# Kernel optimization log

Measured on AMD Instinct MI355X. Metric: run time of the kernel, lower is better.

Reference implementation:

```python
import jax, jax.numpy as jnp
import numpy as np

N_NODES = 50000
N_EDGES = 800000
D = 128
N_GRAPHS = 64
N_CLASSES = 10


def setup_inputs() -> dict:
    key = jax.random.key(0)
    ks = jax.random.split(key, 10)
    x = jax.random.normal(ks[0], (N_NODES, D), dtype=jnp.float32)
    edge_index = jax.random.randint(ks[1], (2, N_EDGES), 0, N_NODES, dtype=jnp.int64)
    batch = jnp.sort(jax.random.randint(ks[2], (N_NODES,), 0, N_GRAPHS, dtype=jnp.int64))
    s = 1.0 / np.sqrt(D)
    W1a = jax.random.uniform(ks[3], (D, D), jnp.float32, -s, s)
    W1b = jax.random.uniform(ks[4], (D, D), jnp.float32, -s, s)
    W2a = jax.random.uniform(ks[5], (D, D), jnp.float32, -s, s)
    W2b = jax.random.uniform(ks[6], (D, D), jnp.float32, -s, s)
    Wfc = jax.random.uniform(ks[7], (D, N_CLASSES), jnp.float32, -s, s)
    return {
        "x": x, "edge_index": edge_index, "batch": batch,
        "W1a": W1a, "b1a": jnp.zeros((D,), jnp.float32),
        "W1b": W1b, "b1b": jnp.zeros((D,), jnp.float32),
        "W2a": W2a, "b2a": jnp.zeros((D,), jnp.float32),
        "W2b": W2b, "b2b": jnp.zeros((D,), jnp.float32),
        "Wfc": Wfc, "bfc": jnp.zeros((N_CLASSES,), jnp.float32),
    }


def _gin_conv(x, src, dst, Wa, ba, Wb, bb):
    # sum aggregation of neighbor messages x[src] into dst (eps = 0)
    agg = jax.ops.segment_sum(x[src], dst, num_segments=N_NODES)
    h = x + agg  # (1 + eps) * x + sum_{j->i} x_j
    h = jax.nn.relu(h @ Wa + ba)
    h = jax.nn.relu(h @ Wb + bb)
    return h


def reference(x, edge_index, batch, W1a, b1a, W1b, b1b, W2a, b2a, W2b, b2b, Wfc, bfc):
    src, dst = edge_index[0], edge_index[1]
    h = _gin_conv(x, src, dst, W1a, b1a, W1b, b1b)
    h = _gin_conv(h, src, dst, W2a, b2a, W2b, b2b)
    # global mean pool over graphs
    sums = jax.ops.segment_sum(h, batch, num_segments=N_GRAPHS)
    counts = jax.ops.segment_sum(jnp.ones((h.shape[0], 1), h.dtype), batch, num_segments=N_GRAPHS)
    pooled = sums / jnp.maximum(counts, 1.0)
    logits = pooled @ Wfc + bfc
    return jax.nn.sigmoid(logits)
```

## Files before the change

kernel.cpp:

```cpp
#include <hip/hip_runtime.h>

#define NN 50000
#define NE 800000
#define DF 128
#define NG 64
#define NC 10
#define NBK 98
#define PART_CHUNK 4096
#define PART_GRID 196
#define ACAP 12288
#define FINE_CAP 12288
#define RT 136

typedef short bf16x8 __attribute__((ext_vector_type(8)));
typedef float f32x4  __attribute__((ext_vector_type(4)));

__device__ __forceinline__ void atomAddF(float* p, float v) {
  __hip_atomic_fetch_add(p, v, __ATOMIC_RELAXED, __HIP_MEMORY_SCOPE_AGENT);
}
__device__ __forceinline__ float b2f(unsigned short u) {
  union { unsigned int i; float f; } v; v.i = (unsigned int)u << 16; return v.f;
}
__device__ __forceinline__ unsigned int f2b(float f) {
  unsigned int i = __float_as_uint(f);
  return (i + 0x7fffu + ((i >> 16) & 1u)) >> 16;
}

__global__ __launch_bounds__(256) void k_cast(const float* __restrict__ x,
                                              unsigned short* __restrict__ xb)
{
  const int i = blockIdx.x * 256 + threadIdx.x;
  if (i * 4 >= NN * DF) return;
  const float4 v = reinterpret_cast<const float4*>(x)[i];
  uint2 o;
  o.x = f2b(v.x) | (f2b(v.y) << 16);
  o.y = f2b(v.z) | (f2b(v.w) << 16);
  reinterpret_cast<uint2*>(xb)[i] = o;
}

__global__ __launch_bounds__(256) void k_prepw(const float* __restrict__ W0,
                                               const float* __restrict__ W1,
                                               const float* __restrict__ W2,
                                               const float* __restrict__ W3,
                                               unsigned short* __restrict__ Wt)
{
  const int o = blockIdx.x * 256 + threadIdx.x;
  if (o >= 4 * 2048) return;
  const int mat = o >> 11;
  const float* W = (mat == 0) ? W0 : (mat == 1) ? W1 : (mat == 2) ? W2 : W3;
  const int rem = o & 2047;
  const int kb = rem >> 7;
  const int n  = rem & 127;
  unsigned int u[8];
#pragma unroll
  for (int j = 0; j < 8; ++j) u[j] = f2b(W[(size_t)(kb * 8 + j) * DF + n]);
  uint4 p;
  p.x = u[0] | (u[1] << 16);
  p.y = u[2] | (u[3] << 16);
  p.z = u[4] | (u[5] << 16);
  p.w = u[6] | (u[7] << 16);
  *reinterpret_cast<uint4*>(Wt + (size_t)mat * DF * DF + (size_t)rem * 8) = p;
}

__global__ __launch_bounds__(256) void k_part(const int* __restrict__ src,
                                              const int* __restrict__ dst,
                                              int* __restrict__ cnt_b,
                                              unsigned int* __restrict__ arena)
{
  __shared__ unsigned int stage[PART_CHUNK];
  __shared__ int lhist[128], lcnt[128], lcur[128], gbase[128];
  const int tid = threadIdx.x;
  const int e0  = blockIdx.x * PART_CHUNK;
  const int nE  = min(PART_CHUNK, NE - e0);

  for (int i = tid; i < 128; i += 256) lhist[i] = 0;
  __syncthreads();

  unsigned int pk[16];
  int bk[16];
#pragma unroll
  for (int i = 0; i < 16; ++i) {
    const int e = e0 + i * 256 + tid;
    if (e < NE) {
      const int d = dst[e];
      const int s = src[e];
      const int b = d >> 9;
      bk[i] = b;
      pk[i] = ((unsigned int)b << 25) | ((unsigned int)(d & 511) << 16) | (unsigned int)s;
      atomicAdd(&lhist[b], 1);
    } else {
      bk[i] = -1;
    }
  }
  __syncthreads();
  for (int i = tid; i < 128; i += 256) lcnt[i] = lhist[i];
  __syncthreads();
  for (int off = 1; off < 128; off <<= 1) {
    int v = 0;
    if (tid < 128 && tid >= off) v = lhist[tid - off];
    __syncthreads();
    if (tid < 128) lhist[tid] += v;
    __syncthreads();
  }
  if (tid < 128) lcur[tid] = lhist[tid] - lcnt[tid];
  __syncthreads();
#pragma unroll
  for (int i = 0; i < 16; ++i) {
    if (bk[i] >= 0) {
      const int pos = atomicAdd(&lcur[bk[i]], 1);
      stage[pos] = pk[i];
    }
  }
  __syncthreads();
  if (tid < NBK) {
    const int c = lcnt[tid];
    if (c > 0) gbase[tid] = atomicAdd(&cnt_b[tid], c);
  }
  __syncthreads();
  for (int idx = tid; idx < nE; idx += 256) {
    const unsigned int p = stage[idx];
    const int b = (int)(p >> 25);
    const int loff = lhist[b] - lcnt[b];
    arena[(size_t)b * ACAP + gbase[b] + (idx - loff)] = p;
  }
}

__global__ __launch_bounds__(128) void k_bscan(const int* __restrict__ cnt_b,
                                               int* __restrict__ base_b,
                                               int* __restrict__ rs)
{
  __shared__ int sm[128];
  const int t = threadIdx.x;
  const int v = (t < NBK) ? cnt_b[t] : 0;
  sm[t] = v;
  __syncthreads();
  for (int off = 1; off < 128; off <<= 1) {
    int u = (t >= off) ? sm[t - off] : 0;
    __syncthreads();
    sm[t] += u;
    __syncthreads();
  }
  base_b[t] = sm[t] - v;
  if (t == NBK - 1) rs[NN] = sm[t];
}

__global__ __launch_bounds__(256) void k_fine(const unsigned int* __restrict__ arena,
                                              const int* __restrict__ cnt_b,
                                              const int* __restrict__ base_b,
                                              int* __restrict__ rs,
                                              unsigned short* __restrict__ es)
{
  __shared__ unsigned short les[FINE_CAP];
  __shared__ int bins[4096];
  __shared__ int partials[256];
  const int tid   = threadIdx.x;
  const int b     = blockIdx.x;
  const int cnt   = cnt_b[b];
  const int wbase = base_b[b];
  const int nbase = b << 9;
  const int nwin  = min(512, NN - nbase);
  const unsigned int* ap = arena + (size_t)b * ACAP;

  for (int i = tid; i < 4096; i += 256) bins[i] = 0;
  __syncthreads();
  for (int idx = tid; idx < cnt; idx += 256) {
    const unsigned int p = ap[idx];
    const int key = (int)(((p >> 16) & 511) << 3) | (int)((p & 0xffffu) >> 13);
    atomicAdd(&bins[key], 1);
  }
  __syncthreads();
  const int b16 = tid * 16;
  int sum = 0;
#pragma unroll
  for (int k = 0; k < 16; ++k) sum += bins[b16 + k];
  partials[tid] = sum;
  __syncthreads();
  for (int off = 1; off < 256; off <<= 1) {
    int u = (tid >= off) ? partials[tid - off] : 0;
    __syncthreads();
    partials[tid] += u;
    __syncthreads();
  }
  int run = partials[tid] - sum;
#pragma unroll
  for (int k = 0; k < 16; ++k) {
    const int v = bins[b16 + k];
    bins[b16 + k] = run;
    run += v;
  }
  __syncthreads();
  for (int i = tid; i < nwin; i += 256) rs[nbase + i] = wbase + bins[i << 3];
  __syncthreads();
  if (cnt <= FINE_CAP) {
    for (int idx = tid; idx < cnt; idx += 256) {
      const unsigned int p = ap[idx];
      const int key = (int)(((p >> 16) & 511) << 3) | (int)((p & 0xffffu) >> 13);
      const int pos = atomicAdd(&bins[key], 1);
      les[pos] = (unsigned short)(p & 0xffffu);
    }
    __syncthreads();
    for (int i = tid; i < cnt; i += 256) es[wbase + i] = les[i];
  } else {
    for (int idx = tid; idx < cnt; idx += 256) {
      const unsigned int p = ap[idx];
      const int key = (int)(((p >> 16) & 511) << 3) | (int)((p & 0xffffu) >> 13);
      const int pos = atomicAdd(&bins[key], 1);
      es[wbase + pos] = (unsigned short)(p & 0xffffu);
    }
  }
}

__global__ __launch_bounds__(256) void k_gather(const unsigned short* __restrict__ feat,
                                                unsigned short* __restrict__ outp,
                                                const int* __restrict__ rs,
                                                const unsigned short* __restrict__ es)
{
  const int wid  = (blockIdx.x * 256 + threadIdx.x) >> 6;
  const int lane = threadIdx.x & 63;
  if (wid >= NN) return;
  const int beg = rs[wid];
  const int end = rs[wid + 1];
  const int off = lane * 2;

  const unsigned int self = *reinterpret_cast<const unsigned int*>(feat + (size_t)wid * DF + off);
  float ax = b2f(self & 0xffff), ay = b2f(self >> 16);
  int j = beg;
  while (j < end && (j & 3)) {
    const int s = es[j];
    const unsigned int u = *reinterpret_cast<const unsigned int*>(feat + (size_t)s * DF + off);
    ax += b2f(u & 0xffff);
    ay += b2f(u >> 16);
    ++j;
  }
  for (; j + 3 < end; j += 4) {
    const uint2 e4 = *reinterpret_cast<const uint2*>(es + j);
    const int s0 = (int)(e4.x & 0xffffu), s1 = (int)(e4.x >> 16);
    const int s2 = (int)(e4.y & 0xffffu), s3 = (int)(e4.y >> 16);
    const unsigned int u0 = *reinterpret_cast<const unsigned int*>(feat + (size_t)s0 * DF + off);
    const unsigned int u1 = *reinterpret_cast<const unsigned int*>(feat + (size_t)s1 * DF + off);
    const unsigned int u2 = *reinterpret_cast<const unsigned int*>(feat + (size_t)s2 * DF + off);
    const unsigned int u3 = *reinterpret_cast<const unsigned int*>(feat + (size_t)s3 * DF + off);
    ax += b2f(u0 & 0xffff) + b2f(u1 & 0xffff) + b2f(u2 & 0xffff) + b2f(u3 & 0xffff);
    ay += b2f(u0 >> 16)    + b2f(u1 >> 16)    + b2f(u2 >> 16)    + b2f(u3 >> 16);
  }
  for (; j < end; ++j) {
    const int s = es[j];
    const unsigned int u = *reinterpret_cast<const unsigned int*>(feat + (size_t)s * DF + off);
    ax += b2f(u & 0xffff);
    ay += b2f(u >> 16);
  }
  const unsigned int o = f2b(ax) | (f2b(ay) << 16);
  *reinterpret_cast<unsigned int*>(outp + (size_t)wid * DF + off) = o;
}

__global__ __launch_bounds__(512) void k_gemm2(const unsigned short* __restrict__ Ab,
                                               const unsigned short* __restrict__ Wta,
                                               const float* __restrict__ ba,
                                               const unsigned short* __restrict__ Wtb,
                                               const float* __restrict__ bb,
                                               unsigned short* __restrict__ outb, int M)
{
  __shared__ unsigned short WbL[2048 * 8];
  __shared__ unsigned short hL[8][16 * RT];
  const int tid  = threadIdx.x;
  const int lane = tid & 63;
  const int w    = tid >> 6;
  const int col  = lane & 15;
  const int kq   = lane >> 4;

  for (int i = tid; i < 2048; i += 512)
    *reinterpret_cast<uint4*>(&WbL[i * 8]) =
        *reinterpret_cast<const uint4*>(&Wtb[(size_t)i * 8]);

  bf16x8 wfa[8][4];
#pragma unroll
  for (int nf = 0; nf < 8; ++nf)
#pragma unroll
    for (int s = 0; s < 4; ++s)
      wfa[nf][s] = *reinterpret_cast<const bf16x8*>(
          Wta + ((size_t)(s * 4 + kq) * 128 + nf * 16 + col) * 8);

  float4 bva[8], bvb[8];
#pragma unroll
  for (int nf = 0; nf < 8; ++nf) {
    bva[nf] = *reinterpret_cast<const float4*>(ba + nf * 16 + kq * 4);
    bvb[nf] = *reinterpret_cast<const float4*>(bb + nf * 16 + kq * 4);
  }

  __syncthreads();

  unsigned short* hw = &hL[w][0];
  const int m   = blockIdx.x * 128 + w * 16 + col;
  const int mld = (m < M) ? m : (M - 1);

  bf16x8 bc[4];
#pragma unroll
  for (int s = 0; s < 4; ++s)
    bc[s] = *reinterpret_cast<const bf16x8*>(Ab + (size_t)mld * DF + s * 32 + kq * 8);

  f32x4 acc[8];
#pragma unroll
  for (int nf = 0; nf < 8; ++nf) acc[nf] = (f32x4){0.f, 0.f, 0.f, 0.f};
#pragma unroll
  for (int s = 0; s < 4; ++s)
#pragma unroll
    for (int nf = 0; nf < 8; ++nf)
      acc[nf] = __builtin_amdgcn_mfma_f32_16x16x32_bf16(wfa[nf][s], bc[s], acc[nf], 0, 0, 0);

#pragma unroll
  for (int nf = 0; nf < 8; ++nf) {
    uint2 pk;
    pk.x = f2b(fmaxf(acc[nf][0] + bva[nf].x, 0.f)) | (f2b(fmaxf(acc[nf][1] + bva[nf].y, 0.f)) << 16);
    pk.y = f2b(fmaxf(acc[nf][2] + bva[nf].z, 0.f)) | (f2b(fmaxf(acc[nf][3] + bva[nf].w, 0.f)) << 16);
    *reinterpret_cast<uint2*>(&hw[col * RT + nf * 16 + kq * 4]) = pk;
  }
  asm volatile("s_waitcnt lgkmcnt(0)" ::: "memory");
  __builtin_amdgcn_sched_barrier(0);

  f32x4 acc2[8];
#pragma unroll
  for (int nf = 0; nf < 8; ++nf) acc2[nf] = (f32x4){0.f, 0.f, 0.f, 0.f};
#pragma unroll
  for (int s = 0; s < 4; ++s) {
    const bf16x8 hb = *reinterpret_cast<const bf16x8*>(&hw[col * RT + s * 32 + kq * 8]);
#pragma unroll
    for (int nf = 0; nf < 8; ++nf) {
      const bf16x8 wb = *reinterpret_cast<const bf16x8*>(
          &WbL[((s * 4 + kq) * 128 + nf * 16 + col) * 8]);
      acc2[nf] = __builtin_amdgcn_mfma_f32_16x16x32_bf16(wb, hb, acc2[nf], 0, 0, 0);
    }
  }
  if (m < M) {
#pragma unroll
    for (int nf = 0; nf < 8; ++nf) {
      ushort4 p;
      p.x = (unsigned short)f2b(fmaxf(acc2[nf][0] + bvb[nf].x, 0.f));
      p.y = (unsigned short)f2b(fmaxf(acc2[nf][1] + bvb[nf].y, 0.f));
      p.z = (unsigned short)f2b(fmaxf(acc2[nf][2] + bvb[nf].z, 0.f));
      p.w = (unsigned short)f2b(fmaxf(acc2[nf][3] + bvb[nf].w, 0.f));
      *reinterpret_cast<ushort4*>(outb + (size_t)m * DF + nf * 16 + kq * 4) = p;
    }
  }
}

__global__ __launch_bounds__(256) void k_pool(const unsigned short* __restrict__ h,
                                              const int* __restrict__ batch,
                                              float* __restrict__ sums,
                                              int* __restrict__ cnts)
{
  const int wv   = (blockIdx.x * 256 + threadIdx.x) >> 6;
  const int lane = threadIdx.x & 63;
  const int n0 = wv * 32;
  if (n0 >= NN) return;
  const int n1 = min(n0 + 32, NN);
  const int off = lane * 2;

  const int gfirst = batch[n0];
  const int glast  = batch[n1 - 1];
  float ax = 0.f, ay = 0.f;

  if (gfirst == glast) {
#pragma unroll 4
    for (int i = n0; i < n1; ++i) {
      const unsigned int u = *reinterpret_cast<const unsigned int*>(h + (size_t)i * DF + off);
      ax += b2f(u & 0xffff);
      ay += b2f(u >> 16);
    }
    atomAddF(&sums[gfirst * DF + off],     ax);
    atomAddF(&sums[gfirst * DF + off + 1], ay);
    if (lane == 0) atomicAdd(&cnts[gfirst], n1 - n0);
  } else {
    int g = gfirst, cnt = 0;
    for (int i = n0; i < n1; ++i) {
      const int gi = batch[i];
      if (gi != g) {
        atomAddF(&sums[g * DF + off],     ax);
        atomAddF(&sums[g * DF + off + 1], ay);
        if (lane == 0) atomicAdd(&cnts[g], cnt);
        ax = 0.f; ay = 0.f; cnt = 0; g = gi;
      }
      const unsigned int u = *reinterpret_cast<const unsigned int*>(h + (size_t)i * DF + off);
      ax += b2f(u & 0xffff);
      ay += b2f(u >> 16);
      ++cnt;
    }
    atomAddF(&sums[g * DF + off],     ax);
    atomAddF(&sums[g * DF + off + 1], ay);
    if (lane == 0) atomicAdd(&cnts[g], cnt);
  }
}

__global__ __launch_bounds__(256) void k_head(const float* __restrict__ sums,
                                              const int* __restrict__ cnts,
                                              const float* __restrict__ Wfc,
                                              const float* __restrict__ bfc,
                                              float* __restrict__ out)
{
  for (int o = threadIdx.x; o < NG * NC; o += 256) {
    const int g = o / NC, c = o % NC;
    const float inv = 1.f / fmaxf((float)cnts[g], 1.f);
    float z = bfc[c];
    for (int k = 0; k < DF; ++k)
      z = fmaf(sums[g * DF + k] * inv, Wfc[k * NC + c], z);
    out[o] = 1.f / (1.f + expf(-z));
  }
}

extern "C" void kernel_launch(void* const* d_in, const int* in_sizes, int n_in,
                              void* d_out, int out_size, void* d_ws, size_t ws_size,
                              hipStream_t stream)
{
  const float* x   = (const float*)d_in[0];
  const int*   ei  = (const int*)d_in[1];
  const int* batch = (const int*)d_in[2];
  const float* W1a = (const float*)d_in[3];
  const float* b1a = (const float*)d_in[4];
  const float* W1b = (const float*)d_in[5];
  const float* b1b = (const float*)d_in[6];
  const float* W2a = (const float*)d_in[7];
  const float* b2a = (const float*)d_in[8];
  const float* W2b = (const float*)d_in[9];
  const float* b2b = (const float*)d_in[10];
  const float* Wfc = (const float*)d_in[11];
  const float* bfc = (const float*)d_in[12];
  float* out = (float*)d_out;

  const int* src = ei;
  const int* dst = ei + NE;

  unsigned short* xb = (unsigned short*)d_ws;
  unsigned short* A  = xb + (size_t)NN * DF;
  unsigned short* H  = A + (size_t)NN * DF;
  unsigned short* Wt = H + (size_t)NN * DF;
  float* sums  = (float*)(Wt + (size_t)4 * DF * DF);
  int*   cnts  = (int*)(sums + NG * DF);
  int*   cnt_b = cnts + 64;
  int*   base_b= cnt_b + 128;
  int*   rs    = base_b + 128;
  unsigned short* es = (unsigned short*)(rs + (NN + 4));
  unsigned int* arena = (unsigned int*)(es + NE);

  unsigned short* Wt1a = Wt;
  unsigned short* Wt1b = Wt + DF * DF;
  unsigned short* Wt2a = Wt + 2 * DF * DF;
  unsigned short* Wt2b = Wt + 3 * DF * DF;

  const int gemm_grid   = (NN + 127) / 128;
  const int gather_grid = (NN * 64 + 255) / 256;
  const int pool_grid   = ((NN + 31) / 32 + 3) / 4;

  k_cast<<<(NN * DF / 4 + 255) / 256, 256, 0, stream>>>(x, xb);
  k_prepw<<<32, 256, 0, stream>>>(W1a, W1b, W2a, W2b, Wt);
  hipMemsetAsync(sums, 0, (size_t)(NG * DF + 64 + 128) * sizeof(float), stream);
  k_part<<<PART_GRID, 256, 0, stream>>>(src, dst, cnt_b, arena);
  k_bscan<<<1, 128, 0, stream>>>(cnt_b, base_b, rs);
  k_fine<<<NBK, 256, 0, stream>>>(arena, cnt_b, base_b, rs, es);

  k_gather<<<gather_grid, 256, 0, stream>>>(xb, A, rs, es);
  k_gemm2<<<gemm_grid, 512, 0, stream>>>(A, Wt1a, b1a, Wt1b, b1b, A, NN);

  k_gather<<<gather_grid, 256, 0, stream>>>(A, H, rs, es);
  k_gemm2<<<gemm_grid, 512, 0, stream>>>(H, Wt2a, b2a, Wt2b, b2b, H, NN);

  k_pool<<<pool_grid, 256, 0, stream>>>(H, batch, sums, cnts);
  k_head<<<1, 256, 0, stream>>>(sums, cnts, Wfc, bfc, out);
}
```

Measured before the change: 191.6 us.

## Merge cast and weight-prep kernels; restructure GEMM for higher occupancy

Result: no change. 192.9 us (+0.7%).

```diff
diff --git a/kernel.cpp b/kernel.cpp
--- a/kernel.cpp
+++ b/kernel.cpp
@@ -11,6 +11,7 @@
 #define ACAP 12288
 #define FINE_CAP 12288
 #define RT 136
+#define CAST_GRID 6250
 
 typedef short bf16x8 __attribute__((ext_vector_type(8)));
 typedef float f32x4  __attribute__((ext_vector_type(4)));
@@ -26,40 +27,39 @@
   return (i + 0x7fffu + ((i >> 16) & 1u)) >> 16;
 }
 
-__global__ __launch_bounds__(256) void k_cast(const float* __restrict__ x,
-                                              unsigned short* __restrict__ xb)
-{
-  const int i = blockIdx.x * 256 + threadIdx.x;
-  if (i * 4 >= NN * DF) return;
-  const float4 v = reinterpret_cast<const float4*>(x)[i];
-  uint2 o;
-  o.x = f2b(v.x) | (f2b(v.y) << 16);
-  o.y = f2b(v.z) | (f2b(v.w) << 16);
-  reinterpret_cast<uint2*>(xb)[i] = o;
-}
-
-__global__ __launch_bounds__(256) void k_prepw(const float* __restrict__ W0,
-                                               const float* __restrict__ W1,
-                                               const float* __restrict__ W2,
-                                               const float* __restrict__ W3,
-                                               unsigned short* __restrict__ Wt)
-{
-  const int o = blockIdx.x * 256 + threadIdx.x;
-  if (o >= 4 * 2048) return;
-  const int mat = o >> 11;
-  const float* W = (mat == 0) ? W0 : (mat == 1) ? W1 : (mat == 2) ? W2 : W3;
-  const int rem = o & 2047;
-  const int kb = rem >> 7;
-  const int n  = rem & 127;
-  unsigned int u[8];
-#pragma unroll
-  for (int j = 0; j < 8; ++j) u[j] = f2b(W[(size_t)(kb * 8 + j) * DF + n]);
-  uint4 p;
-  p.x = u[0] | (u[1] << 16);
-  p.y = u[2] | (u[3] << 16);
-  p.z = u[4] | (u[5] << 16);
-  p.w = u[6] | (u[7] << 16);
-  *reinterpret_cast<uint4*>(Wt + (size_t)mat * DF * DF + (size_t)rem * 8) = p;
+__global__ __launch_bounds__(256) void k_prep(const float* __restrict__ x,
+                                              unsigned short* __restrict__ xb,
+                                              const float* __restrict__ W0,
+                                              const float* __restrict__ W1,
+                                              const float* __restrict__ W2,
+                                              const float* __restrict__ W3,
+                                              unsigned short* __restrict__ Wt)
+{
+  const int b = blockIdx.x;
+  if (b < CAST_GRID) {
+    const int i = b * 256 + threadIdx.x;
+    const float4 v = reinterpret_cast<const float4*>(x)[i];
+    uint2 o;
+    o.x = f2b(v.x) | (f2b(v.y) << 16);
+    o.y = f2b(v.z) | (f2b(v.w) << 16);
+    reinterpret_cast<uint2*>(xb)[i] = o;
+  } else {
+    const int o = (b - CAST_GRID) * 256 + threadIdx.x;
+    const int mat = o >> 11;
+    const float* W = (mat == 0) ? W0 : (mat == 1) ? W1 : (mat == 2) ? W2 : W3;
+    const int rem = o & 2047;
+    const int kb = rem >> 7;
+    const int n  = rem & 127;
+    unsigned int u[8];
+#pragma unroll
+    for (int j = 0; j < 8; ++j) u[j] = f2b(W[(size_t)(kb * 8 + j) * DF + n]);
+    uint4 p;
+    p.x = u[0] | (u[1] << 16);
+    p.y = u[2] | (u[3] << 16);
+    p.z = u[4] | (u[5] << 16);
+    p.w = u[6] | (u[7] << 16);
+    *reinterpret_cast<uint4*>(Wt + (size_t)mat * DF * DF + (size_t)rem * 8) = p;
+  }
 }
 
 __global__ __launch_bounds__(256) void k_part(const int* __restrict__ src,
@@ -253,32 +253,25 @@
   *reinterpret_cast<unsigned int*>(outp + (size_t)wid * DF + off) = o;
 }
 
-__global__ __launch_bounds__(512) void k_gemm2(const unsigned short* __restrict__ Ab,
-                                               const unsigned short* __restrict__ Wta,
-                                               const float* __restrict__ ba,
-                                               const unsigned short* __restrict__ Wtb,
-                                               const float* __restrict__ bb,
-                                               unsigned short* __restrict__ outb, int M)
-{
-  __shared__ unsigned short WbL[2048 * 8];
-  __shared__ unsigned short hL[8][16 * RT];
+__global__ __launch_bounds__(256, 3) void k_gemm2(const unsigned short* __restrict__ Ab,
+                                                  const unsigned short* __restrict__ Wta,
+                                                  const float* __restrict__ ba,
+                                                  const unsigned short* __restrict__ Wtb,
+                                                  const float* __restrict__ bb,
+                                                  unsigned short* __restrict__ outb, int M)
+{
+  __shared__ unsigned short WaL[2048 * 8];
+  __shared__ unsigned short hL[4][16 * RT];
   const int tid  = threadIdx.x;
   const int lane = tid & 63;
   const int w    = tid >> 6;
   const int col  = lane & 15;
   const int kq   = lane >> 4;
 
-  for (int i = tid; i < 2048; i += 512)
-    *reinterpret_cast<uint4*>(&WbL[i * 8]) =
-        *reinterpret_cast<const uint4*>(&Wtb[(size_t)i * 8]);
-
-  bf16x8 wfa[8][4];
-#pragma unroll
-  for (int nf = 0; nf < 8; ++nf)
-#pragma unroll
-    for (int s = 0; s < 4; ++s)
-      wfa[nf][s] = *reinterpret_cast<const bf16x8*>(
-          Wta + ((size_t)(s * 4 + kq) * 128 + nf * 16 + col) * 8);
+#pragma unroll
+  for (int i = 0; i < 8; ++i)
+    *reinterpret_cast<uint4*>(&WaL[(i * 256 + tid) * 8]) =
+        *reinterpret_cast<const uint4*>(&Wta[(size_t)(i * 256 + tid) * 8]);
 
   float4 bva[8], bvb[8];
 #pragma unroll
@@ -287,10 +280,7 @@
     bvb[nf] = *reinterpret_cast<const float4*>(bb + nf * 16 + kq * 4);
   }
 
-  __syncthreads();
-
-  unsigned short* hw = &hL[w][0];
-  const int m   = blockIdx.x * 128 + w * 16 + col;
+  const int m   = blockIdx.x * 64 + w * 16 + col;
   const int mld = (m < M) ? m : (M - 1);
 
   bf16x8 bc[4];
@@ -298,15 +288,22 @@
   for (int s = 0; s < 4; ++s)
     bc[s] = *reinterpret_cast<const bf16x8*>(Ab + (size_t)mld * DF + s * 32 + kq * 8);
 
+  __syncthreads();
+
   f32x4 acc[8];
 #pragma unroll
   for (int nf = 0; nf < 8; ++nf) acc[nf] = (f32x4){0.f, 0.f, 0.f, 0.f};
 #pragma unroll
-  for (int s = 0; s < 4; ++s)
-#pragma unroll
-    for (int nf = 0; nf < 8; ++nf)
-      acc[nf] = __builtin_amdgcn_mfma_f32_16x16x32_bf16(wfa[nf][s], bc[s], acc[nf], 0, 0, 0);
-
+  for (int s = 0; s < 4; ++s) {
+#pragma unroll
+    for (int nf = 0; nf < 8; ++nf) {
+      const bf16x8 wa = *reinterpret_cast<const bf16x8*>(
+          &WaL[((s * 4 + kq) * 128 + nf * 16 + col) * 8]);
+      acc[nf] = __builtin_amdgcn_mfma_f32_16x16x32_bf16(wa, bc[s], acc[nf], 0, 0, 0);
+    }
+  }
+
+  unsigned short* hw = &hL[w][0];
 #pragma unroll
   for (int nf = 0; nf < 8; ++nf) {
     uint2 pk;
@@ -326,7 +323,7 @@
 #pragma unroll
     for (int nf = 0; nf < 8; ++nf) {
       const bf16x8 wb = *reinterpret_cast<const bf16x8*>(
-          &WbL[((s * 4 + kq) * 128 + nf * 16 + col) * 8]);
+          Wtb + ((size_t)(s * 4 + kq) * 128 + nf * 16 + col) * 8);
       acc2[nf] = __builtin_amdgcn_mfma_f32_16x16x32_bf16(wb, hb, acc2[nf], 0, 0, 0);
     }
   }
@@ -445,22 +442,21 @@
   unsigned short* Wt2a = Wt + 2 * DF * DF;
   unsigned short* Wt2b = Wt + 3 * DF * DF;
 
-  const int gemm_grid   = (NN + 127) / 128;
+  const int gemm_grid   = (NN + 63) / 64;
   const int gather_grid = (NN * 64 + 255) / 256;
   const int pool_grid   = ((NN + 31) / 32 + 3) / 4;
 
-  k_cast<<<(NN * DF / 4 + 255) / 256, 256, 0, stream>>>(x, xb);
-  k_prepw<<<32, 256, 0, stream>>>(W1a, W1b, W2a, W2b, Wt);
+  k_prep<<<CAST_GRID + 32, 256, 0, stream>>>(x, xb, W1a, W1b, W2a, W2b, Wt);
   hipMemsetAsync(sums, 0, (size_t)(NG * DF + 64 + 128) * sizeof(float), stream);
   k_part<<<PART_GRID, 256, 0, stream>>>(src, dst, cnt_b, arena);
   k_bscan<<<1, 128, 0, stream>>>(cnt_b, base_b, rs);
   k_fine<<<NBK, 256, 0, stream>>>(arena, cnt_b, base_b, rs, es);
 
   k_gather<<<gather_grid, 256, 0, stream>>>(xb, A, rs, es);
-  k_gemm2<<<gemm_grid, 512, 0, stream>>>(A, Wt1a, b1a, Wt1b, b1b, A, NN);
+  k_gemm2<<<gemm_grid, 256, 0, stream>>>(A, Wt1a, b1a, Wt1b, b1b, A, NN);
 
   k_gather<<<gather_grid, 256, 0, stream>>>(A, H, rs, es);
-  k_gemm2<<<gemm_grid, 512, 0, stream>>>(H, Wt2a, b2a, Wt2b, b2b, H, NN);
+  k_gemm2<<<gemm_grid, 256, 0, stream>>>(H, Wt2a, b2a, Wt2b, b2b, H, NN);
 
   k_pool<<<pool_grid, 256, 0, stream>>>(H, batch, sums, cnts);
   k_head<<<1, 256, 0, stream>>>(sums, cnts, Wfc, bfc, out);
```
